# Optimization experiments

Measured on AMD Instinct MI355X. Metric: run time of the kernel, lower is better.

## Reference

```python
import jax, jax.numpy as jnp
import numpy as np

B, NB, D, H = 16384, 3, 1024, 8
HD = D // H
EPS = 1e-5

def setup_inputs() -> dict:
    key = jax.random.key(0)
    ks = jax.random.split(key, 24)
    w = lambda k, shp: jax.random.normal(k, shp, jnp.float32) * 0.02
    return {
        "x": jax.random.normal(ks[0], (B, NB, D), jnp.float32),
        # nn.MultiheadAttention params
        "in_proj_w": w(ks[1], (3 * D, D)),
        "in_proj_b": jnp.zeros((3 * D,), jnp.float32),
        "out_w": w(ks[2], (D, D)),
        "out_b": jnp.zeros((D,), jnp.float32),
        # weight_generator MLP
        "wg1_w": w(ks[3], (D, D * NB)), "wg1_b": jnp.zeros((D,), jnp.float32),
        "wg2_w": w(ks[4], (D // 2, D)), "wg2_b": jnp.zeros((D // 2,), jnp.float32),
        "wg3_w": w(ks[5], (NB, D // 2)), "wg3_b": jnp.zeros((NB,), jnp.float32),
        # refiner MLP + LayerNorms
        "r1_w": w(ks[6], (2 * D, D)), "r1_b": jnp.zeros((2 * D,), jnp.float32),
        "ln1_g": jnp.ones((2 * D,), jnp.float32), "ln1_b": jnp.zeros((2 * D,), jnp.float32),
        "r2_w": w(ks[7], (D, 2 * D)), "r2_b": jnp.zeros((D,), jnp.float32),
        "ln2_g": jnp.ones((D,), jnp.float32), "ln2_b": jnp.zeros((D,), jnp.float32),
    }

def _layernorm(x, g, b):
    m = jnp.mean(x, axis=-1, keepdims=True)
    v = jnp.mean(jnp.square(x - m), axis=-1, keepdims=True)
    return (x - m) * jax.lax.rsqrt(v + EPS) * g + b

def _forward(x, in_proj_w, in_proj_b, out_w, out_b,
             wg1_w, wg1_b, wg2_w, wg2_b, wg3_w, wg3_b,
             r1_w, r1_b, ln1_g, ln1_b, r2_w, r2_b, ln2_g, ln2_b):
    b = x.shape[0]
    # --- cross (self) attention over the NB branch tokens ---
    qkv = jnp.einsum("bsd,ed->bse", x, in_proj_w) + in_proj_b  # [B, NB, 3D]
    q, k, v = jnp.split(qkv, 3, axis=-1)
    q = q.reshape(b, NB, H, HD)
    k = k.reshape(b, NB, H, HD)
    v = v.reshape(b, NB, H, HD)
    scores = jnp.einsum("bqhd,bkhd->bhqk", q, k) / jnp.sqrt(jnp.float32(HD))
    attn = jax.nn.softmax(scores, axis=-1)
    o = jnp.einsum("bhqk,bkhd->bqhd", attn, v).reshape(b, NB, D)
    attended = jnp.einsum("bsd,ed->bse", o, out_w) + out_b  # [B, NB, D]
    # --- dynamic softmax gate over branches ---
    flat = attended.reshape(b, NB * D)
    h = jax.nn.relu(flat @ wg1_w.T + wg1_b)
    h = jax.nn.relu(h @ wg2_w.T + wg2_b)
    weights = jax.nn.softmax(h @ wg3_w.T + wg3_b, axis=-1)  # [B, NB]
    weighted = jnp.einsum("bsd,bs->bd", attended, weights)  # [B, D]
    # --- refiner (dropout inactive in eval) ---
    h = weighted @ r1_w.T + r1_b
    h = jax.nn.relu(_layernorm(h, ln1_g, ln1_b))
    out = h @ r2_w.T + r2_b
    return _layernorm(out, ln2_g, ln2_b)

def reference(x, in_proj_w, in_proj_b, out_w, out_b,
              wg1_w, wg1_b, wg2_w, wg2_b, wg3_w, wg3_b,
              r1_w, r1_b, ln1_g, ln1_b, r2_w, r2_b, ln2_g, ln2_b):
    return _forward(x, in_proj_w, in_proj_b, out_w, out_b,
                    wg1_w, wg1_b, wg2_w, wg2_b, wg3_w, wg3_b,
                    r1_w, r1_b, ln1_g, ln1_b, r2_w, r2_b, ln2_g, ln2_b)
```

## Files before the change

kernel.cpp:

```cpp
#include <hip/hip_runtime.h>
#include <hip/hip_bf16.h>

#define BB   16384
#define NBR  3
#define DD   1024
#define HH   8
#define HDD  128

typedef __attribute__((ext_vector_type(8))) short short8;
typedef __attribute__((ext_vector_type(4))) float f32x4;

__device__ __forceinline__ float b2f(ushort u) {
    union { unsigned int i; float f; } x; x.i = ((unsigned int)u) << 16; return x.f;
}
__device__ __forceinline__ ushort f2b(float f) {
    union { __hip_bfloat16 h; ushort u; } x; x.h = __float2bfloat16(f); return x.u;
}

__global__ __launch_bounds__(256) void cvt_f32_bf16(const float* __restrict__ in,
                                                    ushort* __restrict__ out, long n) {
    long i = ((long)blockIdx.x * 256 + threadIdx.x) * 4;
    if (i + 4 > n) return;
    float4 v = *reinterpret_cast<const float4*>(in + i);
    unsigned int a = ((unsigned int)f2b(v.x)) | (((unsigned int)f2b(v.y)) << 16);
    unsigned int b = ((unsigned int)f2b(v.z)) | (((unsigned int)f2b(v.w)) << 16);
    uint2 p; p.x = a; p.y = b;
    *reinterpret_cast<uint2*>(out + i) = p;
}

template<int EPI>
__global__ __launch_bounds__(512, 2)
void gemm256(const ushort* __restrict__ A, const ushort* __restrict__ Bt,
             const float* __restrict__ bias, void* __restrict__ Cout,
             int M, int N, int K) {
    extern __shared__ ushort lds[];

    const int tid  = threadIdx.x;
    const int wid  = tid >> 6;
    const int lane = tid & 63;
    const int cpx  = gridDim.x >> 3;
    const int bid  = (blockIdx.x & 7) * cpx + (blockIdx.x >> 3);
    const int nbn  = N >> 8;
    const int bm   = bid / nbn;
    const int bn   = bid % nbn;
    const long m0  = (long)bm * 256;
    const long n0  = (long)bn * 256;
    const int NT   = K >> 6;

    const int srow = tid >> 3;
    const int kel  = (((tid & 7) ^ (srow & 7)) << 3);
    const int widEl = wid * 512;

    const ushort* gA[2][2];
    const ushort* gB[2][2];
    #pragma unroll
    for (int c = 0; c < 2; c++)
        #pragma unroll
        for (int j = 0; j < 2; j++) {
            gA[c][j] = A  + (size_t)(m0 + c * 128 + j * 64 + srow) * K + kel;
            gB[c][j] = Bt + (size_t)(n0 + c * 128 + j * 64 + srow) * K + kel;
        }

    const int wr = wid >> 2, wc = wid & 3;
    const int lm15 = lane & 15;
    int aoff[8];
    #pragma unroll
    for (int m = 0; m < 8; m++) aoff[m] = (wr * 128 + m * 16 + lm15) * 64;
    int boff[4];
    #pragma unroll
    for (int c = 0; c < 4; c++) boff[c] = (wc * 64 + c * 16 + lm15) * 64;
    const int kbr[2] = {
        (((0 << 6) | ((lane >> 4) << 4)) ^ ((lane & 7) << 4)) >> 1,
        (((1 << 6) | ((lane >> 4) << 4)) ^ ((lane & 7) << 4)) >> 1
    };

    f32x4 acc[8][4];
    #pragma unroll
    for (int m = 0; m < 8; m++)
        #pragma unroll
        for (int c = 0; c < 4; c++) { f32x4 z = {0.f, 0.f, 0.f, 0.f}; acc[m][c] = z; }

    short8 af[8], bf[2];

#define STAGE(C, PB, TT) { \
    const ushort* _g0; const ushort* _g1; int _b; \
    if ((C) < 2) { _g0 = gA[(C)][0] + (TT) * 64; _g1 = gA[(C)][1] + (TT) * 64; \
                   _b = (PB) * 16384 + (C) * 8192 + widEl; } \
    else         { _g0 = gB[(C) - 2][0] + (TT) * 64; _g1 = gB[(C) - 2][1] + (TT) * 64; \
                   _b = 32768 + (PB) * 16384 + ((C) - 2) * 8192 + widEl; } \
    __builtin_amdgcn_global_load_lds((const __attribute__((address_space(1))) void*)_g0, \
        (__attribute__((address_space(3))) void*)&lds[_b], 16, 0, 0); \
    __builtin_amdgcn_global_load_lds((const __attribute__((address_space(1))) void*)_g1, \
        (__attribute__((address_space(3))) void*)&lds[_b + 4096], 16, 0, 0); }

#define READ_A(P, KK) { \
    _Pragma("unroll") \
    for (int _m = 0; _m < 8; _m++) \
        af[_m] = *(const short8*)&lds[(P) * 16384 + aoff[_m] + kbr[KK]]; }

#define READ_B2(P, KK, C0) { \
    bf[0] = *(const short8*)&lds[32768 + (P) * 16384 + boff[(C0)] + kbr[KK]]; \
    bf[1] = *(const short8*)&lds[32768 + (P) * 16384 + boff[(C0) + 1] + kbr[KK]]; }

#define MFMA8x2(C0) { \
    _Pragma("unroll") \
    for (int _m = 0; _m < 8; _m++) { \
        acc[_m][(C0)]     = __builtin_amdgcn_mfma_f32_16x16x32_bf16(af[_m], bf[0], acc[_m][(C0)], 0, 0, 0); \
        acc[_m][(C0) + 1] = __builtin_amdgcn_mfma_f32_16x16x32_bf16(af[_m], bf[1], acc[_m][(C0) + 1], 0, 0, 0); } }

#define TILE_STEP(P, T, PRE) { \
     \
    if (PRE) { STAGE(0, (P) ^ 1, (T) + 1); STAGE(1, (P) ^ 1, (T) + 1); \
               STAGE(2, (P) ^ 1, (T) + 1); STAGE(3, (P) ^ 1, (T) + 1); \
               asm volatile("s_waitcnt vmcnt(8)" ::: "memory"); } \
    else     { asm volatile("s_waitcnt vmcnt(0)" ::: "memory"); } \
    __builtin_amdgcn_s_barrier(); \
    asm volatile("" ::: "memory"); \
    __builtin_amdgcn_sched_barrier(0); \
    READ_A(P, 0); \
    READ_B2(P, 0, 0); \
    __builtin_amdgcn_s_setprio(1); MFMA8x2(0); __builtin_amdgcn_s_setprio(0); \
    __builtin_amdgcn_s_barrier(); \
     \
    READ_B2(P, 0, 2); \
    __builtin_amdgcn_s_barrier(); \
    __builtin_amdgcn_s_setprio(1); MFMA8x2(2); __builtin_amdgcn_s_setprio(0); \
    __builtin_amdgcn_s_barrier(); \
     \
    READ_A(P, 1); \
    READ_B2(P, 1, 0); \
    __builtin_amdgcn_s_barrier(); \
    __builtin_amdgcn_s_setprio(1); MFMA8x2(0); __builtin_amdgcn_s_setprio(0); \
    __builtin_amdgcn_s_barrier(); \
     \
    READ_B2(P, 1, 2); \
    __builtin_amdgcn_s_barrier(); \
    __builtin_amdgcn_s_setprio(1); MFMA8x2(2); __builtin_amdgcn_s_setprio(0); \
    __builtin_amdgcn_s_barrier(); }

    STAGE(0, 0, 0); STAGE(1, 0, 0); STAGE(2, 0, 0); STAGE(3, 0, 0);

    int t = 0;
    for (; t + 2 < NT; t += 2) {
        TILE_STEP(0, t, true);
        TILE_STEP(1, t + 1, true);
    }
    TILE_STEP(0, t, true);
    TILE_STEP(1, t + 1, false);

#undef TILE_STEP
#undef MFMA8x2
#undef READ_B2
#undef READ_A
#undef STAGE

    const int l16 = lane >> 4;
    #pragma unroll
    for (int c = 0; c < 4; c++) {
        const long col = n0 + wc * 64 + c * 16 + lm15;
        const float bc = bias[col];
        #pragma unroll
        for (int m = 0; m < 8; m++) {
            const long row = m0 + wr * 128 + m * 16 + l16 * 4;
            #pragma unroll
            for (int j = 0; j < 4; j++) {
                float v = acc[m][c][j] + bc;
                if (EPI == 1) v = v > 0.f ? v : 0.f;
                if (EPI == 2) ((float*)Cout)[(row + j) * (long)N + col] = v;
                else          ((ushort*)Cout)[(row + j) * (long)N + col] = f2b(v);
            }
        }
    }
}

template<int EPI>
__global__ __launch_bounds__(256, 2)
void gemm_bt(const ushort* __restrict__ A, const ushort* __restrict__ Bt,
             const float* __restrict__ bias, void* __restrict__ Cout,
             int M, int N, int K) {
    __shared__ ushort As[128 * 64];
    __shared__ ushort Bs[128 * 64];
    const int tid  = threadIdx.x;
    const int wid  = tid >> 6;
    const int lane = tid & 63;
    const int cpx  = gridDim.x >> 3;
    const int bid  = (blockIdx.x & 7) * cpx + (blockIdx.x >> 3);
    const int nbn  = N >> 7;
    const int bm   = bid / nbn;
    const int bn   = bid % nbn;
    const long m0  = (long)bm * 128;
    const long n0  = (long)bn * 128;

    const int srow = tid >> 3;
    const int scol = (tid & 7) << 3;
    const ushort* gA = A  + (m0 + srow) * (long)K + scol;
    const ushort* gB = Bt + (n0 + srow) * (long)K + scol;

    f32x4 acc[4][4];
    #pragma unroll
    for (int i = 0; i < 4; i++)
        #pragma unroll
        for (int j = 0; j < 4; j++) { f32x4 z = {0.f, 0.f, 0.f, 0.f}; acc[i][j] = z; }

    const int wr = wid >> 1, wc = wid & 1;
    const int kits = K >> 6;

    for (int kt = 0; kt < kits; ++kt) {
        const ushort* pA = gA + kt * 64;
        const ushort* pB = gB + kt * 64;
        #pragma unroll
        for (int i = 0; i < 4; i++) {
            __builtin_amdgcn_global_load_lds(
                (const __attribute__((address_space(1))) void*)(pA + (long)i * 32 * K),
                (__attribute__((address_space(3))) void*)&As[(i * 32 + wid * 8) * 64],
                16, 0, 0);
        }
        #pragma unroll
        for (int i = 0; i < 4; i++) {
            __builtin_amdgcn_global_load_lds(
                (const __attribute__((address_space(1))) void*)(pB + (long)i * 32 * K),
                (__attribute__((address_space(3))) void*)&Bs[(i * 32 + wid * 8) * 64],
                16, 0, 0);
        }
        __syncthreads();
        #pragma unroll
        for (int kk = 0; kk < 2; kk++) {
            const int ko = kk * 32 + (lane >> 4) * 8;
            short8 af[4], bf[4];
            #pragma unroll
            for (int m = 0; m < 4; m++)
                af[m] = *(const short8*)&As[(wr * 64 + m * 16 + (lane & 15)) * 64 + ko];
            #pragma unroll
            for (int n = 0; n < 4; n++)
                bf[n] = *(const short8*)&Bs[(wc * 64 + n * 16 + (lane & 15)) * 64 + ko];
            #pragma unroll
            for (int m = 0; m < 4; m++)
                #pragma unroll
                for (int n = 0; n < 4; n++)
                    acc[m][n] = __builtin_amdgcn_mfma_f32_16x16x32_bf16(af[m], bf[n], acc[m][n], 0, 0, 0);
        }
        __syncthreads();
    }

    #pragma unroll
    for (int n = 0; n < 4; n++) {
        const long c = n0 + wc * 64 + n * 16 + (lane & 15);
        const float bc = bias[c];
        #pragma unroll
        for (int m = 0; m < 4; m++) {
            const long r = m0 + wr * 64 + m * 16 + (lane >> 4) * 4;
            #pragma unroll
            for (int j = 0; j < 4; j++) {
                float v = acc[m][n][j] + bc;
                if (EPI == 1) v = v > 0.f ? v : 0.f;
                if (EPI == 2) ((float*)Cout)[(r + j) * (long)N + c] = v;
                else          ((ushort*)Cout)[(r + j) * (long)N + c] = f2b(v);
            }
        }
    }
}

__global__ __launch_bounds__(256) void attn_kernel(const ushort* __restrict__ qkv,
                                                   ushort* __restrict__ o) {
    const int w    = (blockIdx.x * 256 + threadIdx.x) >> 6;
    const int lane = threadIdx.x & 63;
    const int b = w >> 3, h = w & 7;
    const ushort* base = qkv + (size_t)b * (3 * 3072) + h * HDD + lane * 2;

    float q[3][2], k[3][2], v[3][2];
    #pragma unroll
    for (int i = 0; i < 3; i++) {
        unsigned int qu = *(const unsigned int*)(base + i * 3072);
        unsigned int ku = *(const unsigned int*)(base + i * 3072 + 1024);
        unsigned int vu = *(const unsigned int*)(base + i * 3072 + 2048);
        q[i][0] = b2f((ushort)(qu & 0xffff)); q[i][1] = b2f((ushort)(qu >> 16));
        k[i][0] = b2f((ushort)(ku & 0xffff)); k[i][1] = b2f((ushort)(ku >> 16));
        v[i][0] = b2f((ushort)(vu & 0xffff)); v[i][1] = b2f((ushort)(vu >> 16));
    }

    float s[3][3];
    #pragma unroll
    for (int i = 0; i < 3; i++)
        #pragma unroll
        for (int j = 0; j < 3; j++)
            s[i][j] = q[i][0] * k[j][0] + q[i][1] * k[j][1];

    #pragma unroll
    for (int off = 32; off; off >>= 1)
        #pragma unroll
        for (int i = 0; i < 3; i++)
            #pragma unroll
            for (int j = 0; j < 3; j++)
                s[i][j] += __shfl_xor(s[i][j], off, 64);

    const float sc = 0.08838834764831845f;
    float a[3][3];
    #pragma unroll
    for (int i = 0; i < 3; i++) {
        float l0 = s[i][0] * sc, l1 = s[i][1] * sc, l2 = s[i][2] * sc;
        float mx = fmaxf(fmaxf(l0, l1), l2);
        float e0 = __expf(l0 - mx), e1 = __expf(l1 - mx), e2 = __expf(l2 - mx);
        float inv = 1.f / (e0 + e1 + e2);
        a[i][0] = e0 * inv; a[i][1] = e1 * inv; a[i][2] = e2 * inv;
    }

    ushort* ob = o + (size_t)b * 3072 + h * HDD + lane * 2;
    #pragma unroll
    for (int i = 0; i < 3; i++) {
        float o0 = a[i][0] * v[0][0] + a[i][1] * v[1][0] + a[i][2] * v[2][0];
        float o1 = a[i][0] * v[0][1] + a[i][1] * v[1][1] + a[i][2] * v[2][1];
        unsigned int pk = ((unsigned int)f2b(o0)) | (((unsigned int)f2b(o1)) << 16);
        *(unsigned int*)(ob + i * 1024) = pk;
    }
}

__global__ __launch_bounds__(256) void gate_kernel(const ushort* __restrict__ h2,
                                                   const float* __restrict__ w3,
                                                   const float* __restrict__ b3,
                                                   const ushort* __restrict__ att,
                                                   ushort* __restrict__ weighted) {
    const int gw = (blockIdx.x * 256 + threadIdx.x) >> 6;
    const int lane = threadIdx.x & 63;
    if (gw >= BB) return;

    const ushort* hr = h2 + (size_t)gw * 512 + lane * 8;
    short8 hv = *(const short8*)hr;
    float hf[8];
    #pragma unroll
    for (int d = 0; d < 8; d++) hf[d] = b2f((ushort)hv[d]);

    float dot[3];
    #pragma unroll
    for (int s = 0; s < 3; s++) {
        const float* wr = w3 + s * 512 + lane * 8;
        float4 wa = *(const float4*)wr;
        float4 wb = *(const float4*)(wr + 4);
        dot[s] = hf[0] * wa.x + hf[1] * wa.y + hf[2] * wa.z + hf[3] * wa.w
               + hf[4] * wb.x + hf[5] * wb.y + hf[6] * wb.z + hf[7] * wb.w;
    }
    #pragma unroll
    for (int off = 32; off; off >>= 1)
        #pragma unroll
        for (int s = 0; s < 3; s++) dot[s] += __shfl_xor(dot[s], off, 64);

    float l0 = dot[0] + b3[0], l1 = dot[1] + b3[1], l2 = dot[2] + b3[2];
    float mx = fmaxf(fmaxf(l0, l1), l2);
    float e0 = __expf(l0 - mx), e1 = __expf(l1 - mx), e2 = __expf(l2 - mx);
    float inv = 1.f / (e0 + e1 + e2);
    float w0 = e0 * inv, w1 = e1 * inv, w2 = e2 * inv;

    const ushort* ab = att + (size_t)gw * 3072;
    ushort* wb = weighted + (size_t)gw * 1024;
    #pragma unroll
    for (int i = 0; i < 2; i++) {
        int d0 = (i * 64 + lane) * 8;
        short8 a0 = *(const short8*)(ab + d0);
        short8 a1 = *(const short8*)(ab + 1024 + d0);
        short8 a2 = *(const short8*)(ab + 2048 + d0);
        short8 r;
        #pragma unroll
        for (int d = 0; d < 8; d++) {
            float v = w0 * b2f((ushort)a0[d]) + w1 * b2f((ushort)a1[d]) + w2 * b2f((ushort)a2[d]);
            r[d] = (short)f2b(v);
        }
        *(short8*)(wb + d0) = r;
    }
}

template<int W, int RELU, int OUTBF16>
__global__ __launch_bounds__(256) void ln_kernel(const float* __restrict__ in,
                                                 const float* __restrict__ g,
                                                 const float* __restrict__ bt,
                                                 void* __restrict__ out) {
    constexpr int E = W / 256;
    const int row = blockIdx.x;
    const float* x = in + (size_t)row * W;
    float v[E];
    float s = 0.f;
    #pragma unroll
    for (int e = 0; e < E; e++) { v[e] = x[threadIdx.x + e * 256]; s += v[e]; }

    __shared__ float red1[4], red2[4];
    const int wid = threadIdx.x >> 6, lane = threadIdx.x & 63;
    #pragma unroll
    for (int off = 32; off; off >>= 1) s += __shfl_xor(s, off, 64);
    if (lane == 0) red1[wid] = s;
    __syncthreads();
    const float mean = (red1[0] + red1[1] + red1[2] + red1[3]) / (float)W;

    float q = 0.f;
    #pragma unroll
    for (int e = 0; e < E; e++) { float d = v[e] - mean; q += d * d; }
    #pragma unroll
    for (int off = 32; off; off >>= 1) q += __shfl_xor(q, off, 64);
    if (lane == 0) red2[wid] = q;
    __syncthreads();
    const float var = (red2[0] + red2[1] + red2[2] + red2[3]) / (float)W;
    const float rstd = rsqrtf(var + 1e-5f);

    #pragma unroll
    for (int e = 0; e < E; e++) {
        int c = threadIdx.x + e * 256;
        float o = (v[e] - mean) * rstd * g[c] + bt[c];
        if (RELU) o = o > 0.f ? o : 0.f;
        if (OUTBF16) ((ushort*)out)[(size_t)row * W + c] = f2b(o);
        else         ((float*)out)[(size_t)row * W + c] = o;
    }
}

extern "C" void kernel_launch(void* const* d_in, const int* in_sizes, int n_in,
                              void* d_out, int out_size, void* d_ws, size_t ws_size,
                              hipStream_t stream) {
    const float* x    = (const float*)d_in[0];
    const float* ipw  = (const float*)d_in[1];
    const float* ipb  = (const float*)d_in[2];
    const float* outw = (const float*)d_in[3];
    const float* outb = (const float*)d_in[4];
    const float* wg1w = (const float*)d_in[5];
    const float* wg1b = (const float*)d_in[6];
    const float* wg2w = (const float*)d_in[7];
    const float* wg2b = (const float*)d_in[8];
    const float* wg3w = (const float*)d_in[9];
    const float* wg3b = (const float*)d_in[10];
    const float* r1w  = (const float*)d_in[11];
    const float* r1b  = (const float*)d_in[12];
    const float* ln1g = (const float*)d_in[13];
    const float* ln1b = (const float*)d_in[14];
    const float* r2w  = (const float*)d_in[15];
    const float* r2b  = (const float*)d_in[16];
    const float* ln2g = (const float*)d_in[17];
    const float* ln2b = (const float*)d_in[18];

    char* ws = (char*)d_ws;
    ushort* w_ip  = (ushort*)(ws + 0);
    ushort* w_out = (ushort*)(ws + 6291456);
    ushort* w_g1  = (ushort*)(ws + 8388608);
    ushort* w_g2  = (ushort*)(ws + 14680064);
    ushort* w_r1  = (ushort*)(ws + 15728640);
    ushort* w_r2  = (ushort*)(ws + 19922944);
    char* R1 = ws + 24117248;
    char* R2 = ws + 124780544;

    ushort* xb       = (ushort*)R1;
    ushort* qkv      = (ushort*)R2;
    ushort* o_att    = (ushort*)R1;
    ushort* attended = (ushort*)R2;
    ushort* h1       = (ushort*)(R2 + 100663296);
    ushort* h2       = (ushort*)(R2 + 134217728);
    ushort* weighted = (ushort*)(R2 + 150994944);
    float*  r1out    = (float*)R2;
    ushort* ln1out   = (ushort*)R1;
    float*  r2out    = (float*)(R2 + 184549376);

    (void)hipFuncSetAttribute((const void*)gemm256<0>, hipFuncAttributeMaxDynamicSharedMemorySize, 131072);
    (void)hipFuncSetAttribute((const void*)gemm256<1>, hipFuncAttributeMaxDynamicSharedMemorySize, 131072);
    (void)hipFuncSetAttribute((const void*)gemm256<2>, hipFuncAttributeMaxDynamicSharedMemorySize, 131072);

    cvt_f32_bf16<<<49152, 256, 0, stream>>>(x,    xb,   (long)49152 * 1024);
    cvt_f32_bf16<<<3072,  256, 0, stream>>>(ipw,  w_ip, (long)3072 * 1024);
    cvt_f32_bf16<<<1024,  256, 0, stream>>>(outw, w_out,(long)1024 * 1024);
    cvt_f32_bf16<<<3072,  256, 0, stream>>>(wg1w, w_g1, (long)1024 * 3072);
    cvt_f32_bf16<<<512,   256, 0, stream>>>(wg2w, w_g2, (long)512 * 1024);
    cvt_f32_bf16<<<2048,  256, 0, stream>>>(r1w,  w_r1, (long)2048 * 1024);
    cvt_f32_bf16<<<2048,  256, 0, stream>>>(r2w,  w_r2, (long)1024 * 2048);

    gemm256<0><<<192 * 12, 512, 131072, stream>>>(xb, w_ip, ipb, qkv, 49152, 3072, 1024);
    attn_kernel<<<32768, 256, 0, stream>>>(qkv, o_att);
    gemm256<0><<<192 * 4,  512, 131072, stream>>>(o_att, w_out, outb, attended, 49152, 1024, 1024);
    gemm256<1><<<64 * 4,   512, 131072, stream>>>(attended, w_g1, wg1b, h1, 16384, 1024, 3072);
    gemm_bt<1><<<128 * 4, 256, 0, stream>>>(h1, w_g2, wg2b, h2, 16384, 512, 1024);
    gate_kernel<<<4096, 256, 0, stream>>>(h2, wg3w, wg3b, attended, weighted);
    gemm256<2><<<64 * 8,   512, 131072, stream>>>(weighted, w_r1, r1b, r1out, 16384, 2048, 1024);
    ln_kernel<2048, 1, 1><<<16384, 256, 0, stream>>>(r1out, ln1g, ln1b, ln1out);
    gemm256<2><<<64 * 4,   512, 131072, stream>>>(ln1out, w_r2, r2b, r2out, 16384, 1024, 2048);
    ln_kernel<1024, 0, 0><<<16384, 256, 0, stream>>>(r2out, ln2g, ln2b, d_out);
}
```

Before: 1.005 ms.

## Interleave GEMM prefetch stages and store refiner GEMM outputs as bf16

The GEMM tile loop now issues its four global-to-LDS stage loads one at a time between the MFMA sub-steps instead of all at once, and waits on fewer outstanding loads. The two refiner GEMMs now write bf16 instead of fp32 output. The LayerNorm kernels read bf16 and process contiguous per-thread chunks with vectorized loads and stores. Together these aim to hide load latency and cut memory traffic on the refiner path, at the cost of extra rounding before the LayerNorms. The vmcnt(2) wait has to match the number of loads each STAGE issues, and if it does not, the MFMAs could read stale LDS data.

Measured after the change: 921.8 us. -8.3%, faster.

```diff
diff --git a/kernel.cpp b/kernel.cpp
--- a/kernel.cpp
+++ b/kernel.cpp
@@ -110,9 +110,8 @@
 
 #define TILE_STEP(P, T, PRE) { \
      \
-    if (PRE) { STAGE(0, (P) ^ 1, (T) + 1); STAGE(1, (P) ^ 1, (T) + 1); \
-               STAGE(2, (P) ^ 1, (T) + 1); STAGE(3, (P) ^ 1, (T) + 1); \
-               asm volatile("s_waitcnt vmcnt(8)" ::: "memory"); } \
+    if (PRE) STAGE(0, (P) ^ 1, (T) + 1); \
+    if (PRE) { asm volatile("s_waitcnt vmcnt(2)" ::: "memory"); } \
     else     { asm volatile("s_waitcnt vmcnt(0)" ::: "memory"); } \
     __builtin_amdgcn_s_barrier(); \
     asm volatile("" ::: "memory"); \
@@ -122,17 +121,20 @@
     __builtin_amdgcn_s_setprio(1); MFMA8x2(0); __builtin_amdgcn_s_setprio(0); \
     __builtin_amdgcn_s_barrier(); \
      \
+    if (PRE) STAGE(1, (P) ^ 1, (T) + 1); \
     READ_B2(P, 0, 2); \
     __builtin_amdgcn_s_barrier(); \
     __builtin_amdgcn_s_setprio(1); MFMA8x2(2); __builtin_amdgcn_s_setprio(0); \
     __builtin_amdgcn_s_barrier(); \
      \
+    if (PRE) STAGE(2, (P) ^ 1, (T) + 1); \
     READ_A(P, 1); \
     READ_B2(P, 1, 0); \
     __builtin_amdgcn_s_barrier(); \
     __builtin_amdgcn_s_setprio(1); MFMA8x2(0); __builtin_amdgcn_s_setprio(0); \
     __builtin_amdgcn_s_barrier(); \
      \
+    if (PRE) STAGE(3, (P) ^ 1, (T) + 1); \
     READ_B2(P, 1, 2); \
     __builtin_amdgcn_s_barrier(); \
     __builtin_amdgcn_s_setprio(1); MFMA8x2(2); __builtin_amdgcn_s_setprio(0); \
@@ -368,17 +370,36 @@
 }
 
 template<int W, int RELU, int OUTBF16>
-__global__ __launch_bounds__(256) void ln_kernel(const float* __restrict__ in,
+__global__ __launch_bounds__(256) void ln_kernel(const ushort* __restrict__ in,
                                                  const float* __restrict__ g,
                                                  const float* __restrict__ bt,
                                                  void* __restrict__ out) {
     constexpr int E = W / 256;
     const int row = blockIdx.x;
-    const float* x = in + (size_t)row * W;
+    const ushort* xr = in + (size_t)row * W + threadIdx.x * E;
+
     float v[E];
+    if (E == 8) {
+        uint4 raw = *reinterpret_cast<const uint4*>(xr);
+        const unsigned int* rw = (const unsigned int*)&raw;
+        #pragma unroll
+        for (int p = 0; p < 4; p++) {
+            v[2 * p]     = b2f((ushort)(rw[p] & 0xffff));
+            v[2 * p + 1] = b2f((ushort)(rw[p] >> 16));
+        }
+    } else {
+        uint2 raw = *reinterpret_cast<const uint2*>(xr);
+        const unsigned int* rw = (const unsigned int*)&raw;
+        #pragma unroll
+        for (int p = 0; p < 2; p++) {
+            v[2 * p]     = b2f((ushort)(rw[p] & 0xffff));
+            v[2 * p + 1] = b2f((ushort)(rw[p] >> 16));
+        }
+    }
+
     float s = 0.f;
     #pragma unroll
-    for (int e = 0; e < E; e++) { v[e] = x[threadIdx.x + e * 256]; s += v[e]; }
+    for (int e = 0; e < E; e++) s += v[e];
 
     __shared__ float red1[4], red2[4];
     const int wid = threadIdx.x >> 6, lane = threadIdx.x & 63;
@@ -398,13 +419,27 @@
     const float var = (red2[0] + red2[1] + red2[2] + red2[3]) / (float)W;
     const float rstd = rsqrtf(var + 1e-5f);
 
+    const int c0 = threadIdx.x * E;
+    float o[E];
     #pragma unroll
     for (int e = 0; e < E; e++) {
-        int c = threadIdx.x + e * 256;
-        float o = (v[e] - mean) * rstd * g[c] + bt[c];
-        if (RELU) o = o > 0.f ? o : 0.f;
-        if (OUTBF16) ((ushort*)out)[(size_t)row * W + c] = f2b(o);
-        else         ((float*)out)[(size_t)row * W + c] = o;
+        float ov = (v[e] - mean) * rstd * g[c0 + e] + bt[c0 + e];
+        if (RELU) ov = ov > 0.f ? ov : 0.f;
+        o[e] = ov;
+    }
+    if (OUTBF16) {
+        ushort* op = (ushort*)out + (size_t)row * W + c0;
+        unsigned int pk[E / 2];
+        #pragma unroll
+        for (int p = 0; p < E / 2; p++)
+            pk[p] = ((unsigned int)f2b(o[2 * p])) | (((unsigned int)f2b(o[2 * p + 1])) << 16);
+        if (E == 8) *reinterpret_cast<uint4*>(op) = *(uint4*)pk;
+        else        *reinterpret_cast<uint2*>(op) = *(uint2*)pk;
+    } else {
+        float* op = (float*)out + (size_t)row * W + c0;
+        #pragma unroll
+        for (int p = 0; p < E / 4; p++)
+            reinterpret_cast<float4*>(op)[p] = ((float4*)o)[p];
     }
 }
 
@@ -448,9 +483,9 @@
     ushort* h1       = (ushort*)(R2 + 100663296);
     ushort* h2       = (ushort*)(R2 + 134217728);
     ushort* weighted = (ushort*)(R2 + 150994944);
-    float*  r1out    = (float*)R2;
+    ushort* r1out    = (ushort*)R2;
     ushort* ln1out   = (ushort*)R1;
-    float*  r2out    = (float*)(R2 + 184549376);
+    ushort* r2out    = (ushort*)(R2 + 184549376);
 
     (void)hipFuncSetAttribute((const void*)gemm256<0>, hipFuncAttributeMaxDynamicSharedMemorySize, 131072);
     (void)hipFuncSetAttribute((const void*)gemm256<1>, hipFuncAttributeMaxDynamicSharedMemorySize, 131072);
@@ -470,8 +505,8 @@
     gemm256<1><<<64 * 4,   512, 131072, stream>>>(attended, w_g1, wg1b, h1, 16384, 1024, 3072);
     gemm_bt<1><<<128 * 4, 256, 0, stream>>>(h1, w_g2, wg2b, h2, 16384, 512, 1024);
     gate_kernel<<<4096, 256, 0, stream>>>(h2, wg3w, wg3b, attended, weighted);
-    gemm256<2><<<64 * 8,   512, 131072, stream>>>(weighted, w_r1, r1b, r1out, 16384, 2048, 1024);
+    gemm256<0><<<64 * 8,   512, 131072, stream>>>(weighted, w_r1, r1b, r1out, 16384, 2048, 1024);
     ln_kernel<2048, 1, 1><<<16384, 256, 0, stream>>>(r1out, ln1g, ln1b, ln1out);
-    gemm256<2><<<64 * 4,   512, 131072, stream>>>(ln1out, w_r2, r2b, r2out, 16384, 1024, 2048);
+    gemm256<0><<<64 * 4,   512, 131072, stream>>>(ln1out, w_r2, r2b, r2out, 16384, 1024, 2048);
     ln_kernel<1024, 0, 0><<<16384, 256, 0, stream>>>(r2out, ln2g, ln2b, d_out);
 }
```
